# Kernel optimization log

Hardware: AMD Instinct MI355X
Metric: run time of the kernel (lower is better)

Reference implementation:

```python
import jax, jax.numpy as jnp
import numpy as np

USER = 50000
ITEM = 20000
N = USER + ITEM
LATDIM = 64
GNN_LAYERS = 2
LAM = 0.2  # args.ris_adj_lambda
IMG_DIM = 4096
TXT_DIM = 768
E_MAIN = 2_000_000
E_MODAL = 1_000_000


def setup_inputs() -> dict:
    key = jax.random.key(0)
    ks = jax.random.split(key, 25)
    f32 = jnp.float32
    inp = {
        "image_embedding": jax.random.normal(ks[0], (ITEM, IMG_DIM), f32),
        "text_embedding": jax.random.normal(ks[1], (ITEM, TXT_DIM), f32),
        "adj_rows": jax.random.randint(ks[2], (E_MAIN,), 0, N, jnp.int32),
        "adj_cols": jax.random.randint(ks[3], (E_MAIN,), 0, N, jnp.int32),
        "adj_vals": jax.random.uniform(ks[4], (E_MAIN,), f32),
        "img_rows": jax.random.randint(ks[5], (E_MODAL,), 0, N, jnp.int32),
        "img_cols": jax.random.randint(ks[6], (E_MODAL,), 0, N, jnp.int32),
        "img_vals": jax.random.uniform(ks[7], (E_MODAL,), f32),
        "txt_rows": jax.random.randint(ks[8], (E_MODAL,), 0, N, jnp.int32),
        "txt_cols": jax.random.randint(ks[9], (E_MODAL,), 0, N, jnp.int32),
        "txt_vals": jax.random.uniform(ks[10], (E_MODAL,), f32),
        "u_sh": jax.random.normal(ks[11], (USER, LATDIM), f32) * 0.1,
        "i_sh": jax.random.normal(ks[12], (ITEM, LATDIM), f32) * 0.1,
        "Wi_sh": jax.random.normal(ks[13], (IMG_DIM, LATDIM), f32) * 0.02,
        "bi_sh": jnp.zeros((LATDIM,), f32),
        "Wt_sh": jax.random.normal(ks[14], (TXT_DIM, LATDIM), f32) * 0.02,
        "bt_sh": jnp.zeros((LATDIM,), f32),
        "u_vsp": jax.random.normal(ks[15], (USER, LATDIM), f32) * 0.1,
        "i_vsp": jax.random.normal(ks[16], (ITEM, LATDIM), f32) * 0.1,
        "Wi_vsp": jax.random.normal(ks[17], (IMG_DIM, LATDIM), f32) * 0.02,
        "bi_vsp": jnp.zeros((LATDIM,), f32),
        "u_tsp": jax.random.normal(ks[18], (USER, LATDIM), f32) * 0.1,
        "i_tsp": jax.random.normal(ks[19], (ITEM, LATDIM), f32) * 0.1,
        "Wt_tsp": jax.random.normal(ks[20], (TXT_DIM, LATDIM), f32) * 0.02,
        "bt_tsp": jnp.zeros((LATDIM,), f32),
    }
    return inp


def _spmm(rows, cols, vals, x):
    # sparse COO [N,N] @ dense [N,D]: gather source rows, scale, scatter-add to dest rows
    return jax.ops.segment_sum(vals[:, None] * x[cols], rows, num_segments=N)


def _l2norm(x):
    # F.normalize(x, p=2, dim=1), eps=1e-12
    n = jnp.linalg.norm(x, axis=1, keepdims=True)
    return x / jnp.maximum(n, 1e-12)


def _branch(uE, iE, feats, ar, ac, av, mr, mc, mv):
    base = jnp.concatenate([uE, iE], axis=0)
    e_adj = _spmm(mr, mc, mv, base)                                   # modal graph aggregation
    e = _spmm(ar, ac, av, jnp.concatenate([uE, _l2norm(feats)], 0))   # pass 1: normalized modal feats
    e2 = _spmm(ar, ac, av, jnp.concatenate([e[:USER], iE], 0))        # pass 2: propagated users + id emb
    e = e + e2 + LAM * e_adj
    total = e
    cur = e
    for _ in range(GNN_LAYERS):
        cur = _spmm(ar, ac, av, cur)
        total = total + cur
    return total  # [N, LATDIM]


def reference(image_embedding, text_embedding,
              adj_rows, adj_cols, adj_vals,
              img_rows, img_cols, img_vals,
              txt_rows, txt_cols, txt_vals,
              u_sh, i_sh, Wi_sh, bi_sh, Wt_sh, bt_sh,
              u_vsp, i_vsp, Wi_vsp, bi_vsp,
              u_tsp, i_tsp, Wt_tsp, bt_tsp):
    # trans == 1: Linear feature projections
    img_sh = image_embedding @ Wi_sh + bi_sh
    txt_sh = text_embedding @ Wt_sh + bt_sh
    # shared-modal model (Model_modal_sh.forward_MM)
    ev_sh = _branch(u_sh, i_sh, img_sh, adj_rows, adj_cols, adj_vals, img_rows, img_cols, img_vals)
    et_sh = _branch(u_sh, i_sh, txt_sh, adj_rows, adj_cols, adj_vals, txt_rows, txt_cols, txt_vals)
    sh = jnp.concatenate([ev_sh, et_sh], axis=-1)  # [N, 2*LATDIM]
    # visual-specific model (Model_visual_sp.forward_MM)
    img_sp = image_embedding @ Wi_vsp + bi_vsp
    ev_sp = _branch(u_vsp, i_vsp, img_sp, adj_rows, adj_cols, adj_vals, img_rows, img_cols, img_vals)
    # text-specific model (Model_text_sp.forward_MM)
    txt_sp = text_embedding @ Wt_tsp + bt_tsp
    et_sp = _branch(u_tsp, i_tsp, txt_sp, adj_rows, adj_cols, adj_vals, txt_rows, txt_cols, txt_vals)
    # pack all model outputs into one array: [N, 4*LATDIM]
    return jnp.concatenate([sh, ev_sp, et_sp], axis=-1)
```

## Files before the change

### kernel.cpp

```cpp
#include <hip/hip_runtime.h>

#define USERN 50000
#define ITEMN 20000
#define NN    70000
#define DTOT  256
#define LAMv  0.2f
#define E_MAINN  2000000
#define E_MODALN 1000000
#define B1    64
#define RPB1  1094
#define CAP   96
#define FLUSH 64
#define NBLK1 128
#define SPAN  5

typedef float  v4f  __attribute__((ext_vector_type(4)));
typedef float  v8f  __attribute__((ext_vector_type(8)));
typedef short  v8s  __attribute__((ext_vector_type(8)));
typedef unsigned short v8u __attribute__((ext_vector_type(8)));

__device__ inline unsigned short f2bf(float f) {
    unsigned u = __float_as_uint(f);
    u += 0x7FFFu + ((u >> 16) & 1u);
    return (unsigned short)(u >> 16);
}
__device__ inline v8f bf8f(v8u u) {
    v8f f;
    #pragma unroll
    for (int i = 0; i < 8; ++i) f[i] = __uint_as_float((unsigned)u[i] << 16);
    return f;
}
__device__ inline v8u f8bf(v8f f) {
    v8u u;
    #pragma unroll
    for (int i = 0; i < 8; ++i) u[i] = f2bf(f[i]);
    return u;
}
__device__ inline ushort4 f4bf(float4 f) {
    return make_ushort4(f2bf(f.x), f2bf(f.y), f2bf(f.z), f2bf(f.w));
}

__device__ inline int wave_incl_scan64(int x, int lane) {
    #pragma unroll
    for (int off = 1; off < 64; off <<= 1) {
        int t = __shfl_up(x, off, 64);
        if (lane >= off) x += t;
    }
    return x;
}

__global__ __launch_bounds__(256) void wt_build(
    const float* __restrict__ W0, const float* __restrict__ W1, int K,
    unsigned short* __restrict__ Wtb)
{
    int idx = blockIdx.x * 256 + threadIdx.x;
    if (idx >= 128 * K) return;
    int c = idx / K, k = idx - c * K;
    float v = (c < 64) ? W0[(size_t)k * 64 + c] : W1[(size_t)k * 64 + (c - 64)];
    Wtb[idx] = f2bf(v);
}

#define LDK 40

__global__ __launch_bounds__(256) void gemm_mfma(
    const float* __restrict__ A, int M, int K,
    const unsigned short* __restrict__ Wtb,
    float* __restrict__ P, int blkA, int blkB)
{
    __shared__ __align__(16) unsigned short As[64 * LDK];
    __shared__ __align__(16) unsigned short Ws[128 * LDK];
    const int tid  = threadIdx.x;
    const int row0 = blockIdx.x * 64;
    const int segLen = K >> 1;
    const int k0   = blockIdx.y * segLen;
    const int kend = k0 + segLen;
    float* outP = P + (size_t)blockIdx.y * ITEMN * DTOT;

    const int w   = tid >> 6;
    const int l   = tid & 63;
    const int l16 = l & 15, kg = l >> 4;

    const int sar = tid >> 2, sak = (tid & 3) * 8;
    const int swc = tid >> 1, swk = (tid & 1) * 16;

    v4f acc[8];
    #pragma unroll
    for (int n = 0; n < 8; ++n) acc[n] = (v4f)0.f;

    for (int kt = k0; kt < kend; kt += 32) {
        __syncthreads();
        {
            int arow = row0 + sar; if (arow >= M) arow = M - 1;
            const float* ap = A + (size_t)arow * K + kt + sak;
            float4 a0 = ((const float4*)ap)[0];
            float4 a1 = ((const float4*)ap)[1];
            *(ushort4*)&As[sar * LDK + sak]     = f4bf(a0);
            *(ushort4*)&As[sar * LDK + sak + 4] = f4bf(a1);
            const unsigned short* wp = Wtb + (size_t)swc * K + kt + swk;
            *(uint4*)&Ws[swc * LDK + swk]     = ((const uint4*)wp)[0];
            *(uint4*)&Ws[swc * LDK + swk + 8] = ((const uint4*)wp)[1];
        }
        __syncthreads();

        v8s af = *(const v8s*)&As[(w * 16 + l16) * LDK + kg * 8];
        #pragma unroll
        for (int n = 0; n < 8; ++n) {
            v8s bf = *(const v8s*)&Ws[(n * 16 + l16) * LDK + kg * 8];
            acc[n] = __builtin_amdgcn_mfma_f32_16x16x32_bf16(af, bf, acc[n], 0, 0, 0);
        }
    }

    #pragma unroll
    for (int n = 0; n < 8; ++n) {
        const int col  = n * 16 + l16;
        const int gcol = (col < 64) ? blkA * 64 + col : blkB * 64 + (col - 64);
        #pragma unroll
        for (int r = 0; r < 4; ++r) {
            int row = row0 + w * 16 + kg * 4 + r;
            if (row < M) outP[(size_t)row * DTOT + gcol] = acc[n][r];
        }
    }
}

__global__ __launch_bounds__(256) void build_feats(
    const float* __restrict__ P,
    const float* __restrict__ u_sh, const float* __restrict__ u_vsp, const float* __restrict__ u_tsp,
    const float* __restrict__ i_sh, const float* __restrict__ i_vsp, const float* __restrict__ i_tsp,
    const float* __restrict__ bi_sh, const float* __restrict__ bt_sh,
    const float* __restrict__ bi_vsp, const float* __restrict__ bt_tsp,
    unsigned short* __restrict__ X1b, unsigned short* __restrict__ X2b)
{
    const int n = blockIdx.x;
    const int t = threadIdx.x;
    const int b = t >> 6, k = t & 63;
    if (n < USERN) {
        const float* u = (b < 2) ? u_sh : (b == 2 ? u_vsp : u_tsp);
        X1b[(size_t)n * DTOT + t] = f2bf(u[(size_t)n * 64 + k]);
    } else {
        const int it = n - USERN;
        const size_t SEG = (size_t)ITEMN * DTOT;
        size_t idx = (size_t)it * DTOT + t;
        float f = P[idx] + P[idx + SEG];
        const float* bias = (b == 0) ? bi_sh : (b == 1 ? bt_sh : (b == 2 ? bi_vsp : bt_tsp));
        f += bias[k];
        float s = f * f;
        #pragma unroll
        for (int off = 32; off > 0; off >>= 1) s += __shfl_xor(s, off, 64);
        X1b[(size_t)n * DTOT + t] = f2bf(f / fmaxf(sqrtf(s), 1e-12f));
        const float* p = (b < 2) ? i_sh : (b == 2 ? i_vsp : i_tsp);
        X2b[(size_t)n * DTOT + t] = f2bf(p[(size_t)it * 64 + k]);
    }
}

__global__ __launch_bounds__(256) void bucket_count(
    const int* __restrict__ ar, const int* __restrict__ mir, const int* __restrict__ mtr,
    int* __restrict__ bcount)
{
    const int g = blockIdx.y;
    const int* rows = (g == 0) ? ar : (g == 1 ? mir : mtr);
    const int E = (g == 0) ? E_MAINN : E_MODALN;
    __shared__ int h[B1];
    if (threadIdx.x < B1) h[threadIdx.x] = 0;
    __syncthreads();
    const int chunk = (E + gridDim.x - 1) / gridDim.x;
    const int c0 = blockIdx.x * chunk, c1 = min(c0 + chunk, E);
    for (int i = c0 + threadIdx.x; i < c1; i += 256)
        atomicAdd(&h[rows[i] / RPB1], 1);
    __syncthreads();
    if (threadIdx.x < B1 && h[threadIdx.x])
        atomicAdd(&bcount[g * B1 + threadIdx.x], h[threadIdx.x]);
}

__global__ __launch_bounds__(256) void bucket_base(
    const int* __restrict__ bcount, int* __restrict__ gbase, int* __restrict__ gcnt)
{
    const int g = threadIdx.x >> 6, lane = threadIdx.x & 63;
    if (g < 3) {
        int v = bcount[g * B1 + lane];
        int x = wave_incl_scan64(v, lane);
        gbase[g * (B1 + 1) + lane] = x - v;
        if (lane == 63) gbase[g * (B1 + 1) + B1] = x;
        gcnt[g * B1 + lane] = 0;
    }
}

__global__ __launch_bounds__(256) void radix_a(
    const int* __restrict__ ar,  const int* __restrict__ ac,  const float* __restrict__ av,
    const int* __restrict__ mir, const int* __restrict__ mic, const float* __restrict__ miv,
    const int* __restrict__ mtr, const int* __restrict__ mtc, const float* __restrict__ mtv,
    const int* __restrict__ gbase, int* __restrict__ gcnt,
    uint2* __restrict__ tmpA, uint2* __restrict__ tmpI, uint2* __restrict__ tmpT)
{
    const int g = blockIdx.y;
    const int* rows   = (g == 0) ? ar : (g == 1 ? mir : mtr);
    const int* cols   = (g == 0) ? ac : (g == 1 ? mic : mtc);
    const float* vals = (g == 0) ? av : (g == 1 ? miv : mtv);
    uint2* tmp        = (g == 0) ? tmpA : (g == 1 ? tmpI : tmpT);
    const int E = (g == 0) ? E_MAINN : E_MODALN;
    const int* gb = gbase + g * (B1 + 1);
    int* gc = gcnt + g * B1;

    __shared__ uint2 buf[B1][CAP];
    __shared__ int bcnt_s[B1];
    const int tid = threadIdx.x;
    if (tid < B1) bcnt_s[tid] = 0;
    __syncthreads();

    const int chunk = (E + gridDim.x - 1) / gridDim.x;
    const int c0 = blockIdx.x * chunk, c1 = min(c0 + chunk, E);
    const int b = tid >> 2, sub = tid & 3;
    const int blane = (tid & 63) & ~3;

    for (int base = c0; base < c1; base += 256) {
        int i = base + tid;
        if (i < c1) {
            int r = rows[i];
            int b1 = r / RPB1;
            int rl = r - b1 * RPB1;
            uint2 entry = make_uint2(((unsigned)rl << 17) | (unsigned)cols[i],
                                     __float_as_uint(vals[i]));
            int slot = atomicAdd(&bcnt_s[b1], 1);
            if (slot < CAP) buf[b1][slot] = entry;
            else tmp[gb[b1] + atomicAdd(&gc[b1], 1)] = entry;
        }
        __syncthreads();
        int bc = min(bcnt_s[b], CAP);
        if (bc >= FLUSH) {
            int goff = 0;
            if (sub == 0) goff = gb[b] + atomicAdd(&gc[b], FLUSH);
            goff = __shfl(goff, blane, 64);
            for (int t = sub; t < FLUSH; t += 4)
                tmp[goff + t] = buf[b][t];
            int rem = bc - FLUSH;
            for (int t = sub; t < rem; t += 4)
                buf[b][t] = buf[b][FLUSH + t];
            if (sub == 0) bcnt_s[b] = rem;
        }
        __syncthreads();
    }
    int bc = min(bcnt_s[b], CAP);
    if (bc > 0) {
        int goff = 0;
        if (sub == 0) goff = gb[b] + atomicAdd(&gc[b], bc);
        goff = __shfl(goff, blane, 64);
        for (int t = sub; t < bc; t += 4)
            tmp[goff + t] = buf[b][t];
    }
}

__global__ __launch_bounds__(256) void bucket_sort(
    const int* __restrict__ gbase,
    const uint2* __restrict__ tmp, uint2* __restrict__ ev, int* __restrict__ rp, int gidx)
{
    const int b1 = blockIdx.x;
    const int r0 = b1 * RPB1;
    const int r1 = min(r0 + RPB1, NN);
    const int nr = r1 - r0;
    const int gb = gbase[gidx * (B1 + 1) + b1];
    const int count = gbase[gidx * (B1 + 1) + b1 + 1] - gb;
    __shared__ int lcnt[RPB1];
    __shared__ int lrp[RPB1];
    __shared__ int wsum[4];
    const int tid = threadIdx.x, lane = tid & 63, wv = tid >> 6;
    for (int t = tid; t < nr; t += 256) lcnt[t] = 0;
    __syncthreads();
    for (int t = tid; t < count; t += 256)
        atomicAdd(&lcnt[tmp[gb + t].x >> 17], 1);
    __syncthreads();
    int loc[SPAN]; int s = 0;
    #pragma unroll
    for (int j = 0; j < SPAN; ++j) {
        int idx = tid * SPAN + j;
        int v = (idx < nr) ? lcnt[idx] : 0;
        loc[j] = s; s += v;
    }
    int x = wave_incl_scan64(s, lane);
    if (lane == 63) wsum[wv] = x;
    __syncthreads();
    int woff = 0;
    for (int i = 0; i < wv; ++i) woff += wsum[i];
    int ex = woff + x - s;
    #pragma unroll
    for (int j = 0; j < SPAN; ++j) {
        int idx = tid * SPAN + j;
        if (idx < nr) lrp[idx] = gb + ex + loc[j];
    }
    __syncthreads();
    for (int t = tid; t < nr; t += 256) rp[r0 + t] = lrp[t];
    if (tid == 0 && r1 == NN) rp[NN] = gb + count;
    __syncthreads();
    int t = tid;
    for (; t + 768 < count; t += 1024) {
        uint2 q0 = tmp[gb + t];
        uint2 q1 = tmp[gb + t + 256];
        uint2 q2 = tmp[gb + t + 512];
        uint2 q3 = tmp[gb + t + 768];
        int p0 = atomicAdd(&lrp[q0.x >> 17], 1);
        int p1 = atomicAdd(&lrp[q1.x >> 17], 1);
        int p2 = atomicAdd(&lrp[q2.x >> 17], 1);
        int p3 = atomicAdd(&lrp[q3.x >> 17], 1);
        ev[p0] = make_uint2(q0.x & 0x1FFFFu, q0.y);
        ev[p1] = make_uint2(q1.x & 0x1FFFFu, q1.y);
        ev[p2] = make_uint2(q2.x & 0x1FFFFu, q2.y);
        ev[p3] = make_uint2(q3.x & 0x1FFFFu, q3.y);
    }
    for (; t < count; t += 256) {
        uint2 q = tmp[gb + t];
        int p = atomicAdd(&lrp[q.x >> 17], 1);
        ev[p] = make_uint2(q.x & 0x1FFFFu, q.y);
    }
}

#define SPMM8_HEAD                                                                  \
    const int w = (blockIdx.x * blockDim.x + threadIdx.x) >> 6;                     \
    if (w >= NN) return;                                                            \
    const int lane = threadIdx.x & 63;                                              \
    const int half = lane >> 5, l5 = lane & 31;                                     \
    const v8u* __restrict__ Xv = (const v8u*)Xb;                                    \
    int e = rp[w]; const int end = rp[w + 1];                                       \
    v8f acc = (v8f)0.f;                                                             \
    for (; e + 8 <= end; e += 8) {                                                  \
        uint2 q0 = ev[e + half],     q1 = ev[e + 2 + half];                         \
        uint2 q2 = ev[e + 4 + half], q3 = ev[e + 6 + half];                         \
        v8f g0 = bf8f(Xv[(size_t)q0.x * 32 + l5]);                                  \
        v8f g1 = bf8f(Xv[(size_t)q1.x * 32 + l5]);                                  \
        v8f g2 = bf8f(Xv[(size_t)q2.x * 32 + l5]);                                  \
        v8f g3 = bf8f(Xv[(size_t)q3.x * 32 + l5]);                                  \
        float v0 = __uint_as_float(q0.y), v1 = __uint_as_float(q1.y);               \
        float v2 = __uint_as_float(q2.y), v3 = __uint_as_float(q3.y);               \
        _Pragma("unroll")                                                           \
        for (int i = 0; i < 8; ++i) {                                               \
            acc[i] = fmaf(v0, g0[i], acc[i]); acc[i] = fmaf(v1, g1[i], acc[i]);     \
            acc[i] = fmaf(v2, g2[i], acc[i]); acc[i] = fmaf(v3, g3[i], acc[i]);     \
        }                                                                           \
    }                                                                               \
    for (; e + 2 <= end; e += 2) {                                                  \
        uint2 q = ev[e + half];                                                     \
        v8f g = bf8f(Xv[(size_t)q.x * 32 + l5]);                                    \
        float v = __uint_as_float(q.y);                                             \
        _Pragma("unroll")                                                           \
        for (int i = 0; i < 8; ++i) acc[i] = fmaf(v, g[i], acc[i]);                 \
    }                                                                               \
    if (e < end && half == 0) {                                                     \
        uint2 q = ev[e];                                                            \
        v8f g = bf8f(Xv[(size_t)q.x * 32 + l5]);                                    \
        float v = __uint_as_float(q.y);                                             \
        _Pragma("unroll")                                                           \
        for (int i = 0; i < 8; ++i) acc[i] = fmaf(v, g[i], acc[i]);                 \
    }                                                                               \
    _Pragma("unroll")                                                               \
    for (int i = 0; i < 8; ++i) acc[i] += __shfl_xor(acc[i], 32, 64);               \
    if (half != 0) return;                                                          \
    const size_t oidx = (size_t)w * DTOT + l5 * 8;

__global__ __launch_bounds__(256) void spmm_e1(
    const int* __restrict__ rp, const uint2* __restrict__ ev,
    const unsigned short* __restrict__ Xb, unsigned short* __restrict__ E1b,
    unsigned short* __restrict__ X2b)
{
    SPMM8_HEAD
    v8u ub = f8bf(acc);
    *(v8u*)&E1b[oidx] = ub;
    if (w < USERN) *(v8u*)&X2b[oidx] = ub;
}

__global__ __launch_bounds__(256) void fused_comb_main(
    const int* __restrict__ rp, const uint2* __restrict__ ev,
    const unsigned short* __restrict__ Xb, const unsigned short* __restrict__ E1b,
    float* __restrict__ out)
{
    SPMM8_HEAD
    v8f o = bf8f(*(const v8u*)&E1b[oidx]);
    #pragma unroll
    for (int i = 0; i < 8; ++i) o[i] += acc[i];
    *(v8f*)&out[oidx] = o;
}

__global__ __launch_bounds__(256) void spmm_l1(
    const int* __restrict__ rp, const uint2* __restrict__ ev,
    const unsigned short* __restrict__ Xb, unsigned short* __restrict__ C1b)
{
    SPMM8_HEAD
    *(v8u*)&C1b[oidx] = f8bf(acc);
}

__global__ __launch_bounds__(256) void fused_final(
    const int* __restrict__ rp, const uint2* __restrict__ ev,
    const unsigned short* __restrict__ Xb, float* __restrict__ out)
{
    SPMM8_HEAD
    v8f o = *(const v8f*)&out[oidx];
    v8f c = bf8f(Xv[(size_t)w * 32 + l5]);
    #pragma unroll
    for (int i = 0; i < 8; ++i) o[i] += c[i] + acc[i];
    *(v8f*)&out[oidx] = o;
}

__global__ __launch_bounds__(256) void modal_add(
    const int* __restrict__ rpI, const uint2* __restrict__ evI,
    const int* __restrict__ rpT, const uint2* __restrict__ evT,
    const unsigned short* __restrict__ X1b, const unsigned short* __restrict__ X2b,
    float* __restrict__ out, unsigned short* __restrict__ OUTb)
{
    const int gw = (blockIdx.x * blockDim.x + threadIdx.x) >> 6;
    if (gw >= 2 * NN) return;
    const int r = gw >> 1, m = gw & 1;
    const int lane = threadIdx.x & 63;
    const int qt = lane >> 4, l4 = lane & 15;
    const int* rp   = m ? rpT : rpI;
    const uint2* ev = m ? evT : evI;
    const int slot = m * 8 + (l4 >> 3) * 16 + (l4 & 7);
    const v8u* X1v = (const v8u*)X1b;
    const v8u* X2v = (const v8u*)X2b;
    v8f acc = (v8f)0.f;
    int e = rp[r]; const int end = rp[r + 1];
    for (; e + 4 <= end; e += 4) {
        uint2 q = ev[e + qt];
        const v8u* B = ((int)q.x < USERN) ? X1v : X2v;
        v8f g = bf8f(B[(size_t)q.x * 32 + slot]);
        float v = __uint_as_float(q.y) * LAMv;
        #pragma unroll
        for (int i = 0; i < 8; ++i) acc[i] = fmaf(v, g[i], acc[i]);
    }
    if (qt < end - e) {
        uint2 q = ev[e + qt];
        const v8u* B = ((int)q.x < USERN) ? X1v : X2v;
        v8f g = bf8f(B[(size_t)q.x * 32 + slot]);
        float v = __uint_as_float(q.y) * LAMv;
        #pragma unroll
        for (int i = 0; i < 8; ++i) acc[i] = fmaf(v, g[i], acc[i]);
    }
    #pragma unroll
    for (int i = 0; i < 8; ++i) {
        acc[i] += __shfl_xor(acc[i], 16, 64);
        acc[i] += __shfl_xor(acc[i], 32, 64);
    }
    if (lane < 16) {
        const size_t idx = (size_t)r * DTOT + slot * 8;
        v8f o = *(const v8f*)&out[idx];
        #pragma unroll
        for (int i = 0; i < 8; ++i) o[i] += acc[i];
        *(v8f*)&out[idx] = o;
        *(v8u*)&OUTb[idx] = f8bf(o);
    }
}

extern "C" void kernel_launch(void* const* d_in, const int* in_sizes, int n_in,
                              void* d_out, int out_size, void* d_ws, size_t ws_size,
                              hipStream_t stream)
{
    const float* img = (const float*)d_in[0];
    const float* txt = (const float*)d_in[1];
    const int*   ar  = (const int*)d_in[2];
    const int*   ac  = (const int*)d_in[3];
    const float* av  = (const float*)d_in[4];
    const int*   mir = (const int*)d_in[5];
    const int*   mic = (const int*)d_in[6];
    const float* miv = (const float*)d_in[7];
    const int*   mtr = (const int*)d_in[8];
    const int*   mtc = (const int*)d_in[9];
    const float* mtv = (const float*)d_in[10];
    const float* u_sh   = (const float*)d_in[11];
    const float* i_sh   = (const float*)d_in[12];
    const float* Wi_sh  = (const float*)d_in[13];
    const float* bi_sh  = (const float*)d_in[14];
    const float* Wt_sh  = (const float*)d_in[15];
    const float* bt_sh  = (const float*)d_in[16];
    const float* u_vsp  = (const float*)d_in[17];
    const float* i_vsp  = (const float*)d_in[18];
    const float* Wi_vsp = (const float*)d_in[19];
    const float* bi_vsp = (const float*)d_in[20];
    const float* u_tsp  = (const float*)d_in[21];
    const float* i_tsp  = (const float*)d_in[22];
    const float* Wt_tsp = (const float*)d_in[23];
    const float* bt_tsp = (const float*)d_in[24];

    const size_t NE = (size_t)NN * DTOT;
    unsigned short* X1b  = (unsigned short*)d_ws;
    unsigned short* X2b  = X1b + NE;
    unsigned short* OUTb = X2b + NE;
    unsigned short* E1b  = OUTb + NE;
    unsigned short* C1b  = X1b;
    float* P = (float*)(E1b + NE);
    unsigned short* WtbI = (unsigned short*)(P + 2 * (size_t)ITEMN * DTOT);
    unsigned short* WtbT = WtbI + 128 * 4096;
    uint2* evA  = (uint2*)(WtbT + 128 * 768);
    uint2* evI  = evA + E_MAINN;
    uint2* evT  = evI + E_MODALN;
    uint2* tmpA = evT + E_MODALN;
    uint2* tmpI = tmpA + E_MAINN;
    uint2* tmpT = tmpI + E_MODALN;
    int*   rpA   = (int*)(tmpT + E_MODALN);
    int*   rpI   = rpA + (NN + 4);
    int*   rpT   = rpI + (NN + 4);
    int*   bcount = rpT + (NN + 4);
    int*   gbase  = bcount + 3 * B1;
    int*   gcnt   = gbase + 3 * (B1 + 1);
    float* out   = (float*)d_out;

    const int waveBlocks  = (NN * 64) / 256;
    const int modalBlocks = (2 * NN * 64) / 256;

    hipMemsetAsync(bcount, 0, 3 * B1 * sizeof(int), stream);
    bucket_count<<<dim3(NBLK1, 3), 256, 0, stream>>>(ar, mir, mtr, bcount);
    bucket_base<<<1, 256, 0, stream>>>(bcount, gbase, gcnt);
    radix_a<<<dim3(NBLK1, 3), 256, 0, stream>>>(ar, ac, av, mir, mic, miv, mtr, mtc, mtv,
                                                gbase, gcnt, tmpA, tmpI, tmpT);
    bucket_sort<<<B1, 256, 0, stream>>>(gbase, tmpA, evA, rpA, 0);
    bucket_sort<<<B1, 256, 0, stream>>>(gbase, tmpI, evI, rpI, 1);
    bucket_sort<<<B1, 256, 0, stream>>>(gbase, tmpT, evT, rpT, 2);

    wt_build<<<(128 * 4096 + 255) / 256, 256, 0, stream>>>(Wi_sh, Wi_vsp, 4096, WtbI);
    wt_build<<<(128 * 768  + 255) / 256, 256, 0, stream>>>(Wt_sh, Wt_tsp,  768, WtbT);

    gemm_mfma<<<dim3((ITEMN + 63) / 64, 2), 256, 0, stream>>>(img, ITEMN, 4096, WtbI, P, 0, 2);
    gemm_mfma<<<dim3((ITEMN + 63) / 64, 2), 256, 0, stream>>>(txt, ITEMN,  768, WtbT, P, 1, 3);

    build_feats<<<NN, 256, 0, stream>>>(P, u_sh, u_vsp, u_tsp, i_sh, i_vsp, i_tsp,
                                        bi_sh, bt_sh, bi_vsp, bt_tsp, X1b, X2b);

    spmm_e1<<<waveBlocks, 256, 0, stream>>>(rpA, evA, X1b, E1b, X2b);

    fused_comb_main<<<waveBlocks, 256, 0, stream>>>(rpA, evA, X2b, E1b, out);

    modal_add<<<modalBlocks, 256, 0, stream>>>(rpI, evI, rpT, evT, X1b, X2b, out, OUTb);

    spmm_l1<<<waveBlocks, 256, 0, stream>>>(rpA, evA, OUTb, C1b);

    fused_final<<<waveBlocks, 256, 0, stream>>>(rpA, evA, C1b, out);
}
```

Before: 1.133 ms.

## Fuse main and modal spmm combine into one kernel; merge bucket_sort launches

Merges fused_comb_main and modal_add into a single comb_all kernel. Each wave now computes the main-adjacency spmm plus both modal spmms for one row and writes only the bf16 OUTb intermediate, so the fp32 out read-modify-write passes between stages go away. fused_final now reads OUTb instead of out. The three bucket_sort launches become one 3D grid. The trade-off is a wave with more serial work, lower parallelism in the modal part (one wave per row instead of two), more register pressure, and bf16 rounding of the intermediate sum.

```diff
diff --git a/kernel.cpp b/kernel.cpp
--- a/kernel.cpp
+++ b/kernel.cpp
@@ -250,8 +250,14 @@
 
 __global__ __launch_bounds__(256) void bucket_sort(
     const int* __restrict__ gbase,
-    const uint2* __restrict__ tmp, uint2* __restrict__ ev, int* __restrict__ rp, int gidx)
-{
+    const uint2* __restrict__ tmpA, const uint2* __restrict__ tmpI, const uint2* __restrict__ tmpT,
+    uint2* __restrict__ evA, uint2* __restrict__ evI, uint2* __restrict__ evT,
+    int* __restrict__ rpA, int* __restrict__ rpI, int* __restrict__ rpT)
+{
+    const int gidx = blockIdx.y;
+    const uint2* tmp = (gidx == 0) ? tmpA : (gidx == 1 ? tmpI : tmpT);
+    uint2* ev        = (gidx == 0) ? evA  : (gidx == 1 ? evI  : evT);
+    int* rp          = (gidx == 0) ? rpA  : (gidx == 1 ? rpI  : rpT);
     const int b1 = blockIdx.x;
     const int r0 = b1 * RPB1;
     const int r1 = min(r0 + RPB1, NN);
@@ -311,43 +317,48 @@
     }
 }
 
+#define SPMM8_BODY(RP, EV)                                                          \
+    {                                                                               \
+        int e = RP[w]; const int end = RP[w + 1];                                   \
+        for (; e + 8 <= end; e += 8) {                                              \
+            uint2 q0 = EV[e + half],     q1 = EV[e + 2 + half];                     \
+            uint2 q2 = EV[e + 4 + half], q3 = EV[e + 6 + half];                     \
+            v8f g0 = bf8f(Xv[(size_t)q0.x * 32 + l5]);                              \
+            v8f g1 = bf8f(Xv[(size_t)q1.x * 32 + l5]);                              \
+            v8f g2 = bf8f(Xv[(size_t)q2.x * 32 + l5]);                              \
+            v8f g3 = bf8f(Xv[(size_t)q3.x * 32 + l5]);                              \
+            float v0 = __uint_as_float(q0.y), v1 = __uint_as_float(q1.y);           \
+            float v2 = __uint_as_float(q2.y), v3 = __uint_as_float(q3.y);           \
+            _Pragma("unroll")                                                       \
+            for (int i = 0; i < 8; ++i) {                                           \
+                acc[i] = fmaf(v0, g0[i], acc[i]); acc[i] = fmaf(v1, g1[i], acc[i]); \
+                acc[i] = fmaf(v2, g2[i], acc[i]); acc[i] = fmaf(v3, g3[i], acc[i]); \
+            }                                                                       \
+        }                                                                           \
+        for (; e + 2 <= end; e += 2) {                                              \
+            uint2 q = EV[e + half];                                                 \
+            v8f g = bf8f(Xv[(size_t)q.x * 32 + l5]);                                \
+            float v = __uint_as_float(q.y);                                         \
+            _Pragma("unroll")                                                       \
+            for (int i = 0; i < 8; ++i) acc[i] = fmaf(v, g[i], acc[i]);             \
+        }                                                                           \
+        if (e < end && half == 0) {                                                 \
+            uint2 q = EV[e];                                                        \
+            v8f g = bf8f(Xv[(size_t)q.x * 32 + l5]);                                \
+            float v = __uint_as_float(q.y);                                         \
+            _Pragma("unroll")                                                       \
+            for (int i = 0; i < 8; ++i) acc[i] = fmaf(v, g[i], acc[i]);             \
+        }                                                                           \
+    }
+
 #define SPMM8_HEAD                                                                  \
     const int w = (blockIdx.x * blockDim.x + threadIdx.x) >> 6;                     \
     if (w >= NN) return;                                                            \
     const int lane = threadIdx.x & 63;                                              \
     const int half = lane >> 5, l5 = lane & 31;                                     \
     const v8u* __restrict__ Xv = (const v8u*)Xb;                                    \
-    int e = rp[w]; const int end = rp[w + 1];                                       \
     v8f acc = (v8f)0.f;                                                             \
-    for (; e + 8 <= end; e += 8) {                                                  \
-        uint2 q0 = ev[e + half],     q1 = ev[e + 2 + half];                         \
-        uint2 q2 = ev[e + 4 + half], q3 = ev[e + 6 + half];                         \
-        v8f g0 = bf8f(Xv[(size_t)q0.x * 32 + l5]);                                  \
-        v8f g1 = bf8f(Xv[(size_t)q1.x * 32 + l5]);                                  \
-        v8f g2 = bf8f(Xv[(size_t)q2.x * 32 + l5]);                                  \
-        v8f g3 = bf8f(Xv[(size_t)q3.x * 32 + l5]);                                  \
-        float v0 = __uint_as_float(q0.y), v1 = __uint_as_float(q1.y);               \
-        float v2 = __uint_as_float(q2.y), v3 = __uint_as_float(q3.y);               \
-        _Pragma("unroll")                                                           \
-        for (int i = 0; i < 8; ++i) {                                               \
-            acc[i] = fmaf(v0, g0[i], acc[i]); acc[i] = fmaf(v1, g1[i], acc[i]);     \
-            acc[i] = fmaf(v2, g2[i], acc[i]); acc[i] = fmaf(v3, g3[i], acc[i]);     \
-        }                                                                           \
-    }                                                                               \
-    for (; e + 2 <= end; e += 2) {                                                  \
-        uint2 q = ev[e + half];                                                     \
-        v8f g = bf8f(Xv[(size_t)q.x * 32 + l5]);                                    \
-        float v = __uint_as_float(q.y);                                             \
-        _Pragma("unroll")                                                           \
-        for (int i = 0; i < 8; ++i) acc[i] = fmaf(v, g[i], acc[i]);                 \
-    }                                                                               \
-    if (e < end && half == 0) {                                                     \
-        uint2 q = ev[e];                                                            \
-        v8f g = bf8f(Xv[(size_t)q.x * 32 + l5]);                                    \
-        float v = __uint_as_float(q.y);                                             \
-        _Pragma("unroll")                                                           \
-        for (int i = 0; i < 8; ++i) acc[i] = fmaf(v, g[i], acc[i]);                 \
-    }                                                                               \
+    SPMM8_BODY(rp, ev)                                                              \
     _Pragma("unroll")                                                               \
     for (int i = 0; i < 8; ++i) acc[i] += __shfl_xor(acc[i], 32, 64);               \
     if (half != 0) return;                                                          \
@@ -364,18 +375,6 @@
     if (w < USERN) *(v8u*)&X2b[oidx] = ub;
 }
 
-__global__ __launch_bounds__(256) void fused_comb_main(
-    const int* __restrict__ rp, const uint2* __restrict__ ev,
-    const unsigned short* __restrict__ Xb, const unsigned short* __restrict__ E1b,
-    float* __restrict__ out)
-{
-    SPMM8_HEAD
-    v8f o = bf8f(*(const v8u*)&E1b[oidx]);
-    #pragma unroll
-    for (int i = 0; i < 8; ++i) o[i] += acc[i];
-    *(v8f*)&out[oidx] = o;
-}
-
 __global__ __launch_bounds__(256) void spmm_l1(
     const int* __restrict__ rp, const uint2* __restrict__ ev,
     const unsigned short* __restrict__ Xb, unsigned short* __restrict__ C1b)
@@ -386,63 +385,104 @@
 
 __global__ __launch_bounds__(256) void fused_final(
     const int* __restrict__ rp, const uint2* __restrict__ ev,
-    const unsigned short* __restrict__ Xb, float* __restrict__ out)
+    const unsigned short* __restrict__ Xb, const unsigned short* __restrict__ OUTb,
+    float* __restrict__ out)
 {
     SPMM8_HEAD
-    v8f o = *(const v8f*)&out[oidx];
+    v8f t = bf8f(*(const v8u*)&OUTb[oidx]);
     v8f c = bf8f(Xv[(size_t)w * 32 + l5]);
     #pragma unroll
-    for (int i = 0; i < 8; ++i) o[i] += c[i] + acc[i];
-    *(v8f*)&out[oidx] = o;
-}
-
-__global__ __launch_bounds__(256) void modal_add(
+    for (int i = 0; i < 8; ++i) t[i] += c[i] + acc[i];
+    *(v8f*)&out[oidx] = t;
+}
+
+__global__ __launch_bounds__(256) void comb_all(
+    const int* __restrict__ rpA, const uint2* __restrict__ evA,
     const int* __restrict__ rpI, const uint2* __restrict__ evI,
     const int* __restrict__ rpT, const uint2* __restrict__ evT,
     const unsigned short* __restrict__ X1b, const unsigned short* __restrict__ X2b,
-    float* __restrict__ out, unsigned short* __restrict__ OUTb)
-{
-    const int gw = (blockIdx.x * blockDim.x + threadIdx.x) >> 6;
-    if (gw >= 2 * NN) return;
-    const int r = gw >> 1, m = gw & 1;
+    const unsigned short* __restrict__ E1b, unsigned short* __restrict__ OUTb)
+{
+    const int w = (blockIdx.x * blockDim.x + threadIdx.x) >> 6;
+    if (w >= NN) return;
     const int lane = threadIdx.x & 63;
+    const int half = lane >> 5, l5 = lane & 31;
     const int qt = lane >> 4, l4 = lane & 15;
-    const int* rp   = m ? rpT : rpI;
-    const uint2* ev = m ? evT : evI;
-    const int slot = m * 8 + (l4 >> 3) * 16 + (l4 & 7);
-    const v8u* X1v = (const v8u*)X1b;
-    const v8u* X2v = (const v8u*)X2b;
+    const v8u* __restrict__ X1v = (const v8u*)X1b;
+    const v8u* __restrict__ X2v = (const v8u*)X2b;
+
+    v8f accI = (v8f)0.f, accT = (v8f)0.f;
+    {
+        const int slot = (l4 >> 3) * 16 + (l4 & 7);
+        int e = rpI[w]; const int end = rpI[w + 1];
+        for (; e + 4 <= end; e += 4) {
+            uint2 q = evI[e + qt];
+            const v8u* B = ((int)q.x < USERN) ? X1v : X2v;
+            v8f g = bf8f(B[(size_t)q.x * 32 + slot]);
+            float v = __uint_as_float(q.y) * LAMv;
+            #pragma unroll
+            for (int i = 0; i < 8; ++i) accI[i] = fmaf(v, g[i], accI[i]);
+        }
+        if (qt < end - e) {
+            uint2 q = evI[e + qt];
+            const v8u* B = ((int)q.x < USERN) ? X1v : X2v;
+            v8f g = bf8f(B[(size_t)q.x * 32 + slot]);
+            float v = __uint_as_float(q.y) * LAMv;
+            #pragma unroll
+            for (int i = 0; i < 8; ++i) accI[i] = fmaf(v, g[i], accI[i]);
+        }
+    }
+    {
+        const int slot = 8 + (l4 >> 3) * 16 + (l4 & 7);
+        int e = rpT[w]; const int end = rpT[w + 1];
+        for (; e + 4 <= end; e += 4) {
+            uint2 q = evT[e + qt];
+            const v8u* B = ((int)q.x < USERN) ? X1v : X2v;
+            v8f g = bf8f(B[(size_t)q.x * 32 + slot]);
+            float v = __uint_as_float(q.y) * LAMv;
+            #pragma unroll
+            for (int i = 0; i < 8; ++i) accT[i] = fmaf(v, g[i], accT[i]);
+        }
+        if (qt < end - e) {
+            uint2 q = evT[e + qt];
+            const v8u* B = ((int)q.x < USERN) ? X1v : X2v;
+            v8f g = bf8f(B[(size_t)q.x * 32 + slot]);
+            float v = __uint_as_float(q.y) * LAMv;
+            #pragma unroll
+            for (int i = 0; i < 8; ++i) accT[i] = fmaf(v, g[i], accT[i]);
+        }
+    }
+    #pragma unroll
+    for (int i = 0; i < 8; ++i) {
+        accI[i] += __shfl_xor(accI[i], 16, 64);
+        accI[i] += __shfl_xor(accI[i], 32, 64);
+        accT[i] += __shfl_xor(accT[i], 16, 64);
+        accT[i] += __shfl_xor(accT[i], 32, 64);
+    }
+
     v8f acc = (v8f)0.f;
-    int e = rp[r]; const int end = rp[r + 1];
-    for (; e + 4 <= end; e += 4) {
-        uint2 q = ev[e + qt];
-        const v8u* B = ((int)q.x < USERN) ? X1v : X2v;
-        v8f g = bf8f(B[(size_t)q.x * 32 + slot]);
-        float v = __uint_as_float(q.y) * LAMv;
-        #pragma unroll
-        for (int i = 0; i < 8; ++i) acc[i] = fmaf(v, g[i], acc[i]);
-    }
-    if (qt < end - e) {
-        uint2 q = ev[e + qt];
-        const v8u* B = ((int)q.x < USERN) ? X1v : X2v;
-        v8f g = bf8f(B[(size_t)q.x * 32 + slot]);
-        float v = __uint_as_float(q.y) * LAMv;
-        #pragma unroll
-        for (int i = 0; i < 8; ++i) acc[i] = fmaf(v, g[i], acc[i]);
-    }
+    {
+        const v8u* __restrict__ Xv = X2v;
+        SPMM8_BODY(rpA, evA)
+    }
+    #pragma unroll
+    for (int i = 0; i < 8; ++i) acc[i] += __shfl_xor(acc[i], 32, 64);
+
+    const bool isImg = (l5 < 8) || (l5 >= 16 && l5 < 24);
+    const int src = (l5 < 8) ? l5 : (l5 < 16 ? l5 - 8 : (l5 < 24 ? l5 - 8 : l5 - 16));
+    v8f mod;
     #pragma unroll
     for (int i = 0; i < 8; ++i) {
-        acc[i] += __shfl_xor(acc[i], 16, 64);
-        acc[i] += __shfl_xor(acc[i], 32, 64);
-    }
-    if (lane < 16) {
-        const size_t idx = (size_t)r * DTOT + slot * 8;
-        v8f o = *(const v8f*)&out[idx];
-        #pragma unroll
-        for (int i = 0; i < 8; ++i) o[i] += acc[i];
-        *(v8f*)&out[idx] = o;
-        *(v8u*)&OUTb[idx] = f8bf(o);
-    }
+        float a = __shfl(accI[i], src, 64);
+        float b = __shfl(accT[i], src, 64);
+        mod[i] = isImg ? a : b;
+    }
+    if (half != 0) return;
+    const size_t oidx = (size_t)w * DTOT + l5 * 8;
+    v8f o = bf8f(*(const v8u*)&E1b[oidx]);
+    #pragma unroll
+    for (int i = 0; i < 8; ++i) o[i] += acc[i] + mod[i];
+    *(v8u*)&OUTb[oidx] = f8bf(o);
 }
 
 extern "C" void kernel_launch(void* const* d_in, const int* in_sizes, int n_in,
@@ -498,17 +538,15 @@
     int*   gcnt   = gbase + 3 * (B1 + 1);
     float* out   = (float*)d_out;
 
-    const int waveBlocks  = (NN * 64) / 256;
-    const int modalBlocks = (2 * NN * 64) / 256;
+    const int waveBlocks = (NN * 64) / 256;
 
     hipMemsetAsync(bcount, 0, 3 * B1 * sizeof(int), stream);
     bucket_count<<<dim3(NBLK1, 3), 256, 0, stream>>>(ar, mir, mtr, bcount);
     bucket_base<<<1, 256, 0, stream>>>(bcount, gbase, gcnt);
     radix_a<<<dim3(NBLK1, 3), 256, 0, stream>>>(ar, ac, av, mir, mic, miv, mtr, mtc, mtv,
                                                 gbase, gcnt, tmpA, tmpI, tmpT);
-    bucket_sort<<<B1, 256, 0, stream>>>(gbase, tmpA, evA, rpA, 0);
-    bucket_sort<<<B1, 256, 0, stream>>>(gbase, tmpI, evI, rpI, 1);
-    bucket_sort<<<B1, 256, 0, stream>>>(gbase, tmpT, evT, rpT, 2);
+    bucket_sort<<<dim3(B1, 3), 256, 0, stream>>>(gbase, tmpA, tmpI, tmpT,
+                                                 evA, evI, evT, rpA, rpI, rpT);
 
     wt_build<<<(128 * 4096 + 255) / 256, 256, 0, stream>>>(Wi_sh, Wi_vsp, 4096, WtbI);
     wt_build<<<(128 * 768  + 255) / 256, 256, 0, stream>>>(Wt_sh, Wt_tsp,  768, WtbT);
@@ -521,11 +559,10 @@
 
     spmm_e1<<<waveBlocks, 256, 0, stream>>>(rpA, evA, X1b, E1b, X2b);
 
-    fused_comb_main<<<waveBlocks, 256, 0, stream>>>(rpA, evA, X2b, E1b, out);
-
-    modal_add<<<modalBlocks, 256, 0, stream>>>(rpI, evI, rpT, evT, X1b, X2b, out, OUTb);
+    comb_all<<<waveBlocks, 256, 0, stream>>>(rpA, evA, rpI, evI, rpT, evT,
+                                             X1b, X2b, E1b, OUTb);
 
     spmm_l1<<<waveBlocks, 256, 0, stream>>>(rpA, evA, OUTb, C1b);
 
-    fused_final<<<waveBlocks, 256, 0, stream>>>(rpA, evA, C1b, out);
-}
+    fused_final<<<waveBlocks, 256, 0, stream>>>(rpA, evA, C1b, OUTb, out);
+}
```

Result: faster. 1.047 ms (-7.5%).
